# Kernel optimization log

Hardware: AMD Instinct MI355X
Metric: run time of the kernel (lower is better)

## Reference

```python
import jax, jax.numpy as jnp
import numpy as np

N = 50000
E = 800000
G = 256          # number of graphs in the batch
F_IN = 128
H1, D1 = 12, 32  # conv1: heads, out-per-head (concat -> 384)
H2, D2 = 1, 64   # conv2: single head
NEG_SLOPE = 0.2


def setup_inputs() -> dict:
    key = jax.random.key(0)
    ks = jax.random.split(key, 12)
    x = jax.random.normal(ks[0], (N, F_IN), dtype=jnp.float32)
    edge_index = jax.random.randint(ks[1], (2, E), 0, N, dtype=jnp.int64)
    batch = jnp.sort(jax.random.randint(ks[2], (N,), 0, G, dtype=jnp.int64))
    # conv1 params (Glorot-ish scaling)
    W1 = jax.random.normal(ks[3], (F_IN, H1 * D1), dtype=jnp.float32) * (1.0 / np.sqrt(F_IN))
    att_src1 = jax.random.normal(ks[4], (H1, D1), dtype=jnp.float32) * (1.0 / np.sqrt(D1))
    att_dst1 = jax.random.normal(ks[5], (H1, D1), dtype=jnp.float32) * (1.0 / np.sqrt(D1))
    bias1 = jnp.zeros((H1 * D1,), dtype=jnp.float32)
    # conv2 params
    W2 = jax.random.normal(ks[6], (H1 * D1, H2 * D2), dtype=jnp.float32) * (1.0 / np.sqrt(H1 * D1))
    att_src2 = jax.random.normal(ks[7], (H2, D2), dtype=jnp.float32) * (1.0 / np.sqrt(D2))
    att_dst2 = jax.random.normal(ks[8], (H2, D2), dtype=jnp.float32) * (1.0 / np.sqrt(D2))
    bias2 = jnp.zeros((H2 * D2,), dtype=jnp.float32)
    return {"x": x, "edge_index": edge_index, "batch": batch,
            "W1": W1, "att_src1": att_src1, "att_dst1": att_dst1, "bias1": bias1,
            "W2": W2, "att_src2": att_src2, "att_dst2": att_dst2, "bias2": bias2}


def gat_conv(x, src, dst, W, att_src, att_dst, bias, heads, d_out):
    # x: [N, F] -> h: [N, heads, d_out]
    h = (x @ W).reshape(N, heads, d_out)
    # per-node attention halves: [N, heads]
    a_src = jnp.einsum('nhd,hd->nh', h, att_src)
    a_dst = jnp.einsum('nhd,hd->nh', h, att_dst)
    # per-edge logits (edges include self-loops): [Etot, heads]
    e = jax.nn.leaky_relu(a_src[src] + a_dst[dst], NEG_SLOPE)
    # segment softmax over incoming edges of each destination node
    m = jax.ops.segment_max(e, dst, num_segments=N)          # [N, heads]
    e = jnp.exp(e - m[dst])
    s = jax.ops.segment_sum(e, dst, num_segments=N)          # [N, heads]
    alpha = e / s[dst]
    # weighted aggregation: [N, heads, d_out]
    out = jax.ops.segment_sum(alpha[:, :, None] * h[src], dst, num_segments=N)
    return out.reshape(N, heads * d_out) + bias


def reference(x, edge_index, batch, W1, att_src1, att_dst1, bias1,
              W2, att_src2, att_dst2, bias2):
    # add self-loops (PyG GATConv default add_self_loops=True)
    loops = jnp.arange(N, dtype=edge_index.dtype)
    src = jnp.concatenate([edge_index[0], loops])
    dst = jnp.concatenate([edge_index[1], loops])

    h = jax.nn.relu(gat_conv(x, src, dst, W1, att_src1, att_dst1, bias1, H1, D1))
    h = gat_conv(h, src, dst, W2, att_src2, att_dst2, bias2, H2, D2)

    # global mean pool over graphs
    sums = jax.ops.segment_sum(h, batch, num_segments=G)                 # [G, 64]
    cnts = jax.ops.segment_sum(jnp.ones((N,), h.dtype), batch, num_segments=G)
    return sums / jnp.maximum(cnts, 1.0)[:, None]
```

## Files before the change

### kernel.cpp

```cpp
#include <hip/hip_runtime.h>

#define N_NODES 50000
#define N_EDGES 800000
#define ETOT (N_EDGES + N_NODES)
#define G_GRAPHS 256
#define F_IN 128
#define H1 12
#define D1 32
#define C1 (H1*D1)
#define C2 64
#define NEG 0.2f
#define SCAN_B 1024
#define NBLK_SCAN ((N_NODES + SCAN_B - 1)/SCAN_B)

using bf16x8  = __attribute__((ext_vector_type(8))) short;
using ushort8 = __attribute__((ext_vector_type(8))) unsigned short;
using f32x4   = __attribute__((ext_vector_type(4))) float;

__device__ __forceinline__ float lrelu(float x){ return x > 0.f ? x : NEG*x; }
__device__ __forceinline__ unsigned short f2bf(float f){
  unsigned u = __float_as_uint(f);
  u += 0x7fffu + ((u >> 16) & 1u);
  return (unsigned short)(u >> 16);
}
__device__ __forceinline__ float bf2f(unsigned short h){
  return __uint_as_float(((unsigned)h) << 16);
}

__global__ void cast_x_kernel(const float* __restrict__ x, unsigned short* __restrict__ xb){
  int i = blockIdx.x*blockDim.x + threadIdx.x;
  int base = i*4;
  if (base >= N_NODES*F_IN) return;
  float4 v = *(const float4*)(x + base);
  ushort4 o; o.x=f2bf(v.x); o.y=f2bf(v.y); o.z=f2bf(v.z); o.w=f2bf(v.w);
  *(ushort4*)(xb + base) = o;
}
__global__ void transpose_w_kernel(const float* __restrict__ W, unsigned short* __restrict__ Wt,
                                   int K, int Nc){
  int i = blockIdx.x*blockDim.x + threadIdx.x;
  if (i >= K*Nc) return;
  int n = i / K, k = i % K;
  Wt[i] = f2bf(W[(size_t)k*Nc + n]);
}
__global__ void wab_prep(const float* __restrict__ W1, const float* __restrict__ att_src,
                         const float* __restrict__ att_dst, unsigned short* __restrict__ wAb){
  int i = blockIdx.x*blockDim.x + threadIdx.x;
  if (i >= 32*F_IN) return;
  int c = i >> 7, k = i & 127;
  float v = 0.f;
  if (c < 12){
    #pragma unroll
    for (int dd=0; dd<D1; ++dd) v += W1[(size_t)k*C1 + c*D1 + dd] * att_src[c*D1 + dd];
  } else if (c < 24){
    int h = c - 12;
    #pragma unroll
    for (int dd=0; dd<D1; ++dd) v += W1[(size_t)k*C1 + h*D1 + dd] * att_dst[h*D1 + dd];
  }
  wAb[i] = f2bf(v);
}

template<int BM,int BN,int WM,int WN,bool F32OUT>
__global__ __launch_bounds__(256) void gemm_mfma(const unsigned short* __restrict__ A,
    const unsigned short* __restrict__ Bt, void* __restrict__ Cv,
    int M, int N, int K){
  constexpr int BK = 32;
  __shared__ unsigned short As2[4][BM][8];
  __shared__ unsigned short Bs2[4][BN][8];
  const int tid  = threadIdx.x;
  const int wid  = tid >> 6, lane = tid & 63;
  constexpr int NWX = BN / WN;
  const int wrow = (wid / NWX) * WM, wcol = (wid % NWX) * WN;
  constexpr int MR = WM/16, NR = WN/16;
  const int row0 = blockIdx.x * BM, col0 = blockIdx.y * BN;
  const int r = lane & 15, koct = lane >> 4;
  f32x4 acc[MR][NR];
  #pragma unroll
  for (int m=0;m<MR;m++)
    #pragma unroll
    for (int n=0;n<NR;n++) acc[m][n] = f32x4{0.f,0.f,0.f,0.f};

  for (int k0 = 0; k0 < K; k0 += BK){
    for (int s = tid; s < BM*8; s += 256){
      int rr = s >> 3, cc = (s & 7) * 4;
      int gr = row0 + rr;
      ushort4 v = (gr < M) ? *(const ushort4*)(A + (size_t)gr*K + k0 + cc)
                           : ushort4{0,0,0,0};
      *(ushort4*)(&As2[cc>>3][rr][cc&7]) = v;
    }
    for (int s = tid; s < BN*8; s += 256){
      int rr = s >> 3, cc = (s & 7) * 4;
      ushort4 v = *(const ushort4*)(Bt + (size_t)(col0+rr)*K + k0 + cc);
      *(ushort4*)(&Bs2[cc>>3][rr][cc&7]) = v;
    }
    __syncthreads();
    bf16x8 af[MR], bq[NR];
    #pragma unroll
    for (int m=0;m<MR;m++) af[m] = *(const bf16x8*)(&As2[koct][wrow + m*16 + r][0]);
    #pragma unroll
    for (int n=0;n<NR;n++) bq[n] = *(const bf16x8*)(&Bs2[koct][wcol + n*16 + r][0]);
    #pragma unroll
    for (int m=0;m<MR;m++)
      #pragma unroll
      for (int n=0;n<NR;n++)
        acc[m][n] = __builtin_amdgcn_mfma_f32_16x16x32_bf16(af[m], bq[n], acc[m][n], 0,0,0);
    __syncthreads();
  }
  #pragma unroll
  for (int m=0;m<MR;m++){
    #pragma unroll
    for (int rr=0; rr<4; rr++){
      int grow = row0 + wrow + m*16 + koct*4 + rr;
      if (grow < M){
        #pragma unroll
        for (int n=0;n<NR;n++){
          if constexpr (F32OUT)
            ((float*)Cv)[(size_t)grow*N + col0 + wcol + n*16 + r] = acc[m][n][rr];
          else
            ((unsigned short*)Cv)[(size_t)grow*N + col0 + wcol + n*16 + r] = f2bf(acc[m][n][rr]);
        }
      }
    }
  }
}

__global__ void count_kernel(const int* __restrict__ ei, int* __restrict__ counts){
  int e = blockIdx.x*blockDim.x + threadIdx.x;
  if (e >= ETOT) return;
  int d = (e < N_EDGES) ? ei[N_EDGES + e] : (e - N_EDGES);
  atomicAdd(&counts[d], 1);
}
__global__ __launch_bounds__(SCAN_B) void scan_pass1(const int* __restrict__ counts,
    int* __restrict__ excl, int* __restrict__ bsum){
  __shared__ int sdata[SCAN_B];
  int i = blockIdx.x*SCAN_B + threadIdx.x;
  int v = (i < N_NODES) ? counts[i] : 0;
  sdata[threadIdx.x] = v;
  __syncthreads();
  for (int off=1; off<SCAN_B; off<<=1){
    int t = (threadIdx.x >= off) ? sdata[threadIdx.x-off] : 0;
    __syncthreads();
    sdata[threadIdx.x] += t;
    __syncthreads();
  }
  if (i < N_NODES) excl[i] = sdata[threadIdx.x] - v;
  if (threadIdx.x == SCAN_B-1) bsum[blockIdx.x] = sdata[SCAN_B-1];
}
__global__ void scan_pass2(int* __restrict__ bsum){
  if (threadIdx.x == 0){
    int acc = 0;
    for (int b=0;b<NBLK_SCAN;b++){ int t = bsum[b]; bsum[b] = acc; acc += t; }
  }
}
__global__ void scan_pass3(int* __restrict__ rowptr, const int* __restrict__ bsum,
                           int* __restrict__ cursor){
  int i = blockIdx.x*blockDim.x + threadIdx.x;
  if (i < N_NODES){
    int r = rowptr[i] + bsum[i/SCAN_B];
    rowptr[i] = r; cursor[i] = r;
  }
  if (i == N_NODES) rowptr[N_NODES] = ETOT;
}
__global__ void scatter_kernel(const int* __restrict__ ei, int* __restrict__ cursor,
                               int* __restrict__ csr_src){
  int e = blockIdx.x*blockDim.x + threadIdx.x;
  if (e >= ETOT) return;
  int s, d;
  if (e < N_EDGES){ s = ei[e]; d = ei[N_EDGES + e]; } else { s = d = e - N_EDGES; }
  int slot = atomicAdd(&cursor[d], 1);
  csr_src[slot] = s;
}

__global__ __launch_bounds__(64) void alpha1_kernel(const int* __restrict__ rowptr,
    const int* __restrict__ csr, const float* __restrict__ asd,
    float* __restrict__ alpha){
  int d = blockIdx.x, lane = threadIdx.x;
  int r0 = rowptr[d], r1 = rowptr[d+1], deg = r1 - r0;
  float4 ad0 = *(const float4*)(asd + (size_t)d*32 + 12);
  float4 ad1 = *(const float4*)(asd + (size_t)d*32 + 16);
  float4 ad2 = *(const float4*)(asd + (size_t)d*32 + 20);
  float ad[12] = {ad0.x,ad0.y,ad0.z,ad0.w, ad1.x,ad1.y,ad1.z,ad1.w, ad2.x,ad2.y,ad2.z,ad2.w};

  if (deg <= 64){
    bool act = lane < deg;
    int j = r0 + lane;
    int s = act ? csr[j] : 0;
    float4 s0 = *(const float4*)(asd + (size_t)s*32);
    float4 s1 = *(const float4*)(asd + (size_t)s*32 + 4);
    float4 s2 = *(const float4*)(asd + (size_t)s*32 + 8);
    float as[12] = {s0.x,s0.y,s0.z,s0.w, s1.x,s1.y,s1.z,s1.w, s2.x,s2.y,s2.z,s2.w};
    float w[12];
    #pragma unroll
    for (int h=0; h<12; ++h){
      float l = act ? lrelu(as[h] + ad[h]) : -1e30f;
      float m = l;
      #pragma unroll
      for (int off=32; off; off>>=1) m = fmaxf(m, __shfl_xor(m, off));
      float wv = act ? __expf(l - m) : 0.f;
      float ss = wv;
      #pragma unroll
      for (int off=32; off; off>>=1) ss += __shfl_xor(ss, off);
      w[h] = wv / ss;
    }
    if (act){
      float4 o0 = {w[0],w[1],w[2],w[3]};
      float4 o1 = {w[4],w[5],w[6],w[7]};
      float4 o2 = {w[8],w[9],w[10],w[11]};
      *(float4*)(alpha + (size_t)j*12)     = o0;
      *(float4*)(alpha + (size_t)j*12 + 4) = o1;
      *(float4*)(alpha + (size_t)j*12 + 8) = o2;
    }
  } else {
    float mx[12], ss[12];
    #pragma unroll
    for (int h=0;h<12;h++){ mx[h] = -1e30f; ss[h] = 0.f; }
    for (int j = r0 + lane; j < r1; j += 64){
      int s = csr[j];
      float4 s0 = *(const float4*)(asd + (size_t)s*32);
      float4 s1 = *(const float4*)(asd + (size_t)s*32 + 4);
      float4 s2 = *(const float4*)(asd + (size_t)s*32 + 8);
      float as[12] = {s0.x,s0.y,s0.z,s0.w, s1.x,s1.y,s1.z,s1.w, s2.x,s2.y,s2.z,s2.w};
      #pragma unroll
      for (int h=0;h<12;h++) mx[h] = fmaxf(mx[h], lrelu(as[h] + ad[h]));
    }
    #pragma unroll
    for (int h=0;h<12;h++){
      #pragma unroll
      for (int off=32; off; off>>=1) mx[h] = fmaxf(mx[h], __shfl_xor(mx[h], off));
    }
    for (int j = r0 + lane; j < r1; j += 64){
      int s = csr[j];
      float4 s0 = *(const float4*)(asd + (size_t)s*32);
      float4 s1 = *(const float4*)(asd + (size_t)s*32 + 4);
      float4 s2 = *(const float4*)(asd + (size_t)s*32 + 8);
      float as[12] = {s0.x,s0.y,s0.z,s0.w, s1.x,s1.y,s1.z,s1.w, s2.x,s2.y,s2.z,s2.w};
      float w[12];
      #pragma unroll
      for (int h=0;h<12;h++){ w[h] = __expf(lrelu(as[h]+ad[h]) - mx[h]); ss[h] += w[h]; }
      float4 o0 = {w[0],w[1],w[2],w[3]};
      float4 o1 = {w[4],w[5],w[6],w[7]};
      float4 o2 = {w[8],w[9],w[10],w[11]};
      *(float4*)(alpha + (size_t)j*12)     = o0;
      *(float4*)(alpha + (size_t)j*12 + 4) = o1;
      *(float4*)(alpha + (size_t)j*12 + 8) = o2;
    }
    float inv[12];
    #pragma unroll
    for (int h=0;h<12;h++){
      #pragma unroll
      for (int off=32; off; off>>=1) ss[h] += __shfl_xor(ss[h], off);
      inv[h] = 1.f / ss[h];
    }
    for (int j = r0 + lane; j < r1; j += 64){
      float4 o0 = *(const float4*)(alpha + (size_t)j*12);
      float4 o1 = *(const float4*)(alpha + (size_t)j*12 + 4);
      float4 o2 = *(const float4*)(alpha + (size_t)j*12 + 8);
      o0.x*=inv[0]; o0.y*=inv[1]; o0.z*=inv[2]; o0.w*=inv[3];
      o1.x*=inv[4]; o1.y*=inv[5]; o1.z*=inv[6]; o1.w*=inv[7];
      o2.x*=inv[8]; o2.y*=inv[9]; o2.z*=inv[10]; o2.w*=inv[11];
      *(float4*)(alpha + (size_t)j*12)     = o0;
      *(float4*)(alpha + (size_t)j*12 + 4) = o1;
      *(float4*)(alpha + (size_t)j*12 + 8) = o2;
    }
  }
}

__global__ __launch_bounds__(256) void agg1x_kernel(const int* __restrict__ rowptr,
    const int* __restrict__ csr, const unsigned short* __restrict__ xb,
    const float* __restrict__ alpha, const unsigned short* __restrict__ w1t,
    const float* __restrict__ bias, unsigned short* __restrict__ out1){
  constexpr int ROWE = 6*F_IN + 8;
  __shared__ unsigned short agg[16*ROWE];
  int tid = threadIdx.x;
  int g = tid >> 4, t16 = tid & 15;
  int d = blockIdx.x*16 + g;
  int r0 = rowptr[d], r1 = rowptr[d+1];
  float acc[12][8];
  #pragma unroll
  for (int h=0;h<12;h++)
    #pragma unroll
    for (int i=0;i<8;i++) acc[h][i] = 0.f;

  float4 a0={0,0,0,0}, a1={0,0,0,0}, a2={0,0,0,0};
  ushort8 xv = {0,0,0,0,0,0,0,0};
  if (r0 < r1){
    int s = csr[r0];
    a0 = *(const float4*)(alpha + (size_t)r0*12);
    a1 = *(const float4*)(alpha + (size_t)r0*12 + 4);
    a2 = *(const float4*)(alpha + (size_t)r0*12 + 8);
    xv = *(const ushort8*)(xb + (size_t)s*F_IN + t16*8);
  }
  for (int j = r0; j < r1; ++j){
    float4 c0=a0, c1=a1, c2=a2; ushort8 cx=xv;
    if (j+1 < r1){
      int s = csr[j+1];
      a0 = *(const float4*)(alpha + (size_t)(j+1)*12);
      a1 = *(const float4*)(alpha + (size_t)(j+1)*12 + 4);
      a2 = *(const float4*)(alpha + (size_t)(j+1)*12 + 8);
      xv = *(const ushort8*)(xb + (size_t)s*F_IN + t16*8);
    }
    float xf[8];
    #pragma unroll
    for (int i=0;i<8;i++) xf[i] = bf2f((unsigned short)cx[i]);
    float aw[12] = {c0.x,c0.y,c0.z,c0.w, c1.x,c1.y,c1.z,c1.w, c2.x,c2.y,c2.z,c2.w};
    #pragma unroll
    for (int h=0;h<12;h++)
      #pragma unroll
      for (int i=0;i<8;i++) acc[h][i] += aw[h]*xf[i];
  }

  int wid = tid >> 6, lane = tid & 63;
  int r = lane & 15, q = lane >> 4;
  #pragma unroll
  for (int half = 0; half < 2; ++half){
    if (half) __syncthreads();
    #pragma unroll
    for (int h = 0; h < 6; ++h){
      ushort8 v;
      #pragma unroll
      for (int i=0;i<8;i++) v[i] = f2bf(acc[half*6+h][i]);
      *(ushort8*)(&agg[g*ROWE + h*F_IN + t16*8]) = v;
    }
    __syncthreads();
    for (int t = wid; t < 12; t += 4){
      int h = t >> 1, nb = t & 1;
      int hh = half*6 + h;
      f32x4 c = {0.f,0.f,0.f,0.f};
      #pragma unroll
      for (int kk=0; kk<4; ++kk){
        bf16x8 af = *(const bf16x8*)(&agg[r*ROWE + h*F_IN + kk*32 + q*8]);
        bf16x8 bq = *(const bf16x8*)(w1t + (size_t)(hh*32 + nb*16 + r)*F_IN + kk*32 + q*8);
        c = __builtin_amdgcn_mfma_f32_16x16x32_bf16(af, bq, c, 0,0,0);
      }
      int col = hh*32 + nb*16 + r;
      float bv = bias[col];
      #pragma unroll
      for (int rr=0; rr<4; ++rr){
        int od = blockIdx.x*16 + q*4 + rr;
        out1[(size_t)od*C1 + col] = f2bf(fmaxf(c[rr] + bv, 0.f));
      }
    }
  }
}

__global__ void a2_kernel(const unsigned short* __restrict__ h2,
    const float* __restrict__ att_src, const float* __restrict__ att_dst,
    float* __restrict__ a_src, float* __restrict__ a_dst){
  int n = blockIdx.x*blockDim.x + threadIdx.x;
  if (n >= N_NODES) return;
  const unsigned short* hp = h2 + (size_t)n*C2;
  float s=0.f, d=0.f;
  #pragma unroll
  for (int k4=0;k4<16;k4++){
    ushort4 v = *(const ushort4*)(hp + k4*4);
    int b = k4*4;
    s += bf2f(v.x)*att_src[b] + bf2f(v.y)*att_src[b+1] + bf2f(v.z)*att_src[b+2] + bf2f(v.w)*att_src[b+3];
    d += bf2f(v.x)*att_dst[b] + bf2f(v.y)*att_dst[b+1] + bf2f(v.z)*att_dst[b+2] + bf2f(v.w)*att_dst[b+3];
  }
  a_src[n]=s; a_dst[n]=d;
}

#define AGG2_CH 64
__global__ __launch_bounds__(64) void agg2f_kernel(const int* __restrict__ rowptr,
    const int* __restrict__ csr, const unsigned short* __restrict__ h2,
    const float* __restrict__ asrc, const float* __restrict__ adst,
    const float* __restrict__ bias, const int* __restrict__ batch,
    float* __restrict__ pool){
  int d = blockIdx.x, tid = threadIdx.x;
  int r0 = rowptr[d], r1 = rowptr[d+1];
  float ad = adst[d];
  float m = -1e30f, ss = 0.f;
  for (int j = r0 + tid; j < r1; j += 64){
    float l = lrelu(asrc[csr[j]] + ad);
    float mn = fmaxf(m, l);
    ss = ss*__expf(m - mn) + __expf(l - mn);
    m = mn;
  }
  #pragma unroll
  for (int off=32; off; off>>=1){
    float m2 = __shfl_xor(m, off);
    float s2 = __shfl_xor(ss, off);
    float mn = fmaxf(m, m2);
    ss = ss*__expf(m - mn) + s2*__expf(m2 - mn);
    m = mn;
  }
  float inv = 1.f / ss;
  __shared__ int   s_lds[AGG2_CH];
  __shared__ float red[3][C2];
  int grp = tid >> 4;
  int fb  = (tid & 15) * 4;
  float a0=0.f, a1=0.f, a2=0.f, a3=0.f;
  for (int c0 = r0; c0 < r1; c0 += AGG2_CH){
    int nc = min(AGG2_CH, r1 - c0);
    __syncthreads();
    if (tid < nc) s_lds[tid] = csr[c0 + tid];
    __syncthreads();
    for (int e = grp; e < nc; e += 4){
      int s = s_lds[e];
      float w = __expf(lrelu(asrc[s] + ad) - m);
      ushort4 hv = *(const ushort4*)(h2 + (size_t)s*C2 + fb);
      a0 += w*bf2f(hv.x); a1 += w*bf2f(hv.y); a2 += w*bf2f(hv.z); a3 += w*bf2f(hv.w);
    }
  }
  __syncthreads();
  if (grp > 0){
    float* p = &red[grp-1][fb];
    p[0]=a0; p[1]=a1; p[2]=a2; p[3]=a3;
  }
  __syncthreads();
  if (grp == 0){
    int g = batch[d];
    float4 b4 = *(const float4*)(bias + fb);
    float v0 = (a0 + red[0][fb+0] + red[1][fb+0] + red[2][fb+0])*inv + b4.x;
    float v1 = (a1 + red[0][fb+1] + red[1][fb+1] + red[2][fb+1])*inv + b4.y;
    float v2 = (a2 + red[0][fb+2] + red[1][fb+2] + red[2][fb+2])*inv + b4.z;
    float v3 = (a3 + red[0][fb+3] + red[1][fb+3] + red[2][fb+3])*inv + b4.w;
    atomicAdd(&pool[g*C2 + fb+0], v0);
    atomicAdd(&pool[g*C2 + fb+1], v1);
    atomicAdd(&pool[g*C2 + fb+2], v2);
    atomicAdd(&pool[g*C2 + fb+3], v3);
  }
}

__global__ void cnt_kernel(const int* __restrict__ batch, int* __restrict__ cnt){
  int n = blockIdx.x*blockDim.x + threadIdx.x;
  if (n < N_NODES) atomicAdd(&cnt[batch[n]], 1);
}
__global__ void finalize_kernel(const float* __restrict__ sums, const int* __restrict__ cnt,
                                float* __restrict__ out){
  int i = blockIdx.x*blockDim.x + threadIdx.x;
  if (i >= G_GRAPHS*C2) return;
  int g = i >> 6;
  out[i] = sums[i] / fmaxf((float)cnt[g], 1.f);
}

extern "C" void kernel_launch(void* const* d_in, const int* in_sizes, int n_in,
                              void* d_out, int out_size, void* d_ws, size_t ws_size,
                              hipStream_t stream) {
  const float* x        = (const float*)d_in[0];
  const int*   ei       = (const int*)  d_in[1];
  const int*   batch    = (const int*)  d_in[2];
  const float* W1       = (const float*)d_in[3];
  const float* att_src1 = (const float*)d_in[4];
  const float* att_dst1 = (const float*)d_in[5];
  const float* bias1    = (const float*)d_in[6];
  const float* W2       = (const float*)d_in[7];
  const float* att_src2 = (const float*)d_in[8];
  const float* att_dst2 = (const float*)d_in[9];
  const float* bias2    = (const float*)d_in[10];
  float* out = (float*)d_out;

  char* ws = (char*)d_ws;
  size_t o = 0;
  auto alloc = [&](size_t bytes)->size_t{ size_t r=o; o=(o+bytes+255)&~(size_t)255; return r; };

  size_t xb_o     = alloc((size_t)N_NODES*F_IN*2);
  size_t w1t_o    = alloc((size_t)C1*F_IN*2);
  size_t w2t_o    = alloc((size_t)C2*C1*2);
  size_t wab_o    = alloc((size_t)32*F_IN*2);
  size_t asd_o    = alloc((size_t)N_NODES*32*4);
  size_t out1_o   = alloc((size_t)N_NODES*C1*2);
  size_t h2_o     = alloc((size_t)N_NODES*C2*2);
  size_t asrc2_o  = alloc((size_t)N_NODES*4);
  size_t adst2_o  = alloc((size_t)N_NODES*4);
  size_t alpha1_o = alloc((size_t)ETOT*H1*4);
  size_t zero_beg = o;
  size_t counts_o = alloc((size_t)N_NODES*4);
  size_t pool_o   = alloc((size_t)G_GRAPHS*C2*4);
  size_t cnt_o    = alloc((size_t)G_GRAPHS*4);
  size_t zero_end = o;
  size_t rowptr_o = alloc((size_t)(N_NODES+1)*4);
  size_t bsum_o   = alloc((size_t)NBLK_SCAN*4);
  size_t cursor_o = alloc((size_t)N_NODES*4);
  size_t csr_o    = alloc((size_t)ETOT*4);

  unsigned short* xb    = (unsigned short*)(ws + xb_o);
  unsigned short* w1t   = (unsigned short*)(ws + w1t_o);
  unsigned short* w2t   = (unsigned short*)(ws + w2t_o);
  unsigned short* wab   = (unsigned short*)(ws + wab_o);
  float* asd    = (float*)(ws + asd_o);
  unsigned short* out1b = (unsigned short*)(ws + out1_o);
  unsigned short* h2b   = (unsigned short*)(ws + h2_o);
  float* asrc2  = (float*)(ws + asrc2_o);
  float* adst2  = (float*)(ws + adst2_o);
  float* alpha1 = (float*)(ws + alpha1_o);
  int*   counts = (int*)  (ws + counts_o);
  float* poolf  = (float*)(ws + pool_o);
  int*   cnt    = (int*)  (ws + cnt_o);
  int*   rowptr = (int*)  (ws + rowptr_o);
  int*   bsum   = (int*)  (ws + bsum_o);
  int*   cursor = (int*)  (ws + cursor_o);
  int*   csrsrc = (int*)  (ws + csr_o);

  hipMemsetAsync(ws + zero_beg, 0, zero_end - zero_beg, stream);

  const int TPB = 256;
  int egrid = (ETOT + TPB - 1)/TPB;

  cast_x_kernel<<<(N_NODES*F_IN/4 + TPB-1)/TPB, TPB, 0, stream>>>(x, xb);
  transpose_w_kernel<<<(F_IN*C1 + TPB-1)/TPB, TPB, 0, stream>>>(W1, w1t, F_IN, C1);
  transpose_w_kernel<<<(C1*C2 + TPB-1)/TPB, TPB, 0, stream>>>(W2, w2t, C1, C2);
  wab_prep<<<(32*F_IN + TPB-1)/TPB, TPB, 0, stream>>>(W1, att_src1, att_dst1, wab);

  count_kernel<<<egrid, TPB, 0, stream>>>(ei, counts);
  scan_pass1<<<NBLK_SCAN, SCAN_B, 0, stream>>>(counts, rowptr, bsum);
  scan_pass2<<<1, 64, 0, stream>>>(bsum);
  scan_pass3<<<(N_NODES + TPB)/TPB, TPB, 0, stream>>>(rowptr, bsum, cursor);
  scatter_kernel<<<egrid, TPB, 0, stream>>>(ei, cursor, csrsrc);

  gemm_mfma<128,32,32,32,true><<<dim3((N_NODES+127)/128, 1), 256, 0, stream>>>(xb, wab, asd, N_NODES, 32, F_IN);
  alpha1_kernel<<<N_NODES, 64, 0, stream>>>(rowptr, csrsrc, asd, alpha1);
  agg1x_kernel<<<N_NODES/16, 256, 0, stream>>>(rowptr, csrsrc, xb, alpha1, w1t, bias1, out1b);

  gemm_mfma<128,64,64,32,false><<<dim3((N_NODES+127)/128, 1), 256, 0, stream>>>(out1b, w2t, h2b, N_NODES, C2, C1);
  a2_kernel<<<(N_NODES + TPB-1)/TPB, TPB, 0, stream>>>(h2b, att_src2, att_dst2, asrc2, adst2);
  agg2f_kernel<<<N_NODES, 64, 0, stream>>>(rowptr, csrsrc, h2b, asrc2, adst2, bias2, batch, poolf);

  cnt_kernel<<<(N_NODES + TPB-1)/TPB, TPB, 0, stream>>>(batch, cnt);
  finalize_kernel<<<(G_GRAPHS*C2 + TPB-1)/TPB, TPB, 0, stream>>>(poolf, cnt, out);
}
```

Before: 510.2 us.

## Fuse layer-1 softmax weights into aggregation kernel, dropping alpha buffer

Merges the separate per-edge softmax kernel into the layer-1 aggregation kernel. Each destination node now gets a 32-lane half-wave that computes the max, then produces unnormalized exp weights in LDS chunks of 16 edges. The two 16-lane groups each process alternate edges and are combined by a shuffle, with the 1/sum normalization applied before the MFMA projection. This removes the write and re-read of the ETOT x 12 float alpha array and one kernel launch. In exchange, each edge's source scores are gathered twice and register pressure rises with 512-thread blocks.

```diff
diff --git a/kernel.cpp b/kernel.cpp
--- a/kernel.cpp
+++ b/kernel.cpp
@@ -170,172 +170,140 @@
   csr_src[slot] = s;
 }
 
-__global__ __launch_bounds__(64) void alpha1_kernel(const int* __restrict__ rowptr,
-    const int* __restrict__ csr, const float* __restrict__ asd,
-    float* __restrict__ alpha){
-  int d = blockIdx.x, lane = threadIdx.x;
-  int r0 = rowptr[d], r1 = rowptr[d+1], deg = r1 - r0;
+__global__ __launch_bounds__(512) void agg1f_kernel(const int* __restrict__ rowptr,
+    const int* __restrict__ csr, const unsigned short* __restrict__ xb,
+    const float* __restrict__ asd, const unsigned short* __restrict__ w1t,
+    const float* __restrict__ bias, unsigned short* __restrict__ out1){
+  constexpr int ROWE = 6*F_IN + 8;
+  __shared__ unsigned short agg[16*ROWE];
+  __shared__ float wlds[16][16*12];
+  __shared__ int   slds[16][16];
+
+  const int tid  = threadIdx.x;
+  const int wv   = tid >> 6;
+  const int lane = tid & 63;
+  const int half = lane >> 5;
+  const int t    = lane & 31;
+  const int eh   = t >> 4;
+  const int t16  = t & 15;
+  const int slot = wv*2 + half;
+  const int d    = blockIdx.x*16 + slot;
+  const int r0 = rowptr[d], r1 = rowptr[d+1];
+
   float4 ad0 = *(const float4*)(asd + (size_t)d*32 + 12);
   float4 ad1 = *(const float4*)(asd + (size_t)d*32 + 16);
   float4 ad2 = *(const float4*)(asd + (size_t)d*32 + 20);
   float ad[12] = {ad0.x,ad0.y,ad0.z,ad0.w, ad1.x,ad1.y,ad1.z,ad1.w, ad2.x,ad2.y,ad2.z,ad2.w};
 
-  if (deg <= 64){
-    bool act = lane < deg;
-    int j = r0 + lane;
-    int s = act ? csr[j] : 0;
+  float mx[12];
+  #pragma unroll
+  for (int h=0;h<12;h++) mx[h] = -1e30f;
+  for (int j = r0 + t; j < r1; j += 32){
+    int s = csr[j];
     float4 s0 = *(const float4*)(asd + (size_t)s*32);
     float4 s1 = *(const float4*)(asd + (size_t)s*32 + 4);
     float4 s2 = *(const float4*)(asd + (size_t)s*32 + 8);
     float as[12] = {s0.x,s0.y,s0.z,s0.w, s1.x,s1.y,s1.z,s1.w, s2.x,s2.y,s2.z,s2.w};
-    float w[12];
-    #pragma unroll
-    for (int h=0; h<12; ++h){
-      float l = act ? lrelu(as[h] + ad[h]) : -1e30f;
-      float m = l;
-      #pragma unroll
-      for (int off=32; off; off>>=1) m = fmaxf(m, __shfl_xor(m, off));
-      float wv = act ? __expf(l - m) : 0.f;
-      float ss = wv;
-      #pragma unroll
-      for (int off=32; off; off>>=1) ss += __shfl_xor(ss, off);
-      w[h] = wv / ss;
-    }
-    if (act){
-      float4 o0 = {w[0],w[1],w[2],w[3]};
-      float4 o1 = {w[4],w[5],w[6],w[7]};
-      float4 o2 = {w[8],w[9],w[10],w[11]};
-      *(float4*)(alpha + (size_t)j*12)     = o0;
-      *(float4*)(alpha + (size_t)j*12 + 4) = o1;
-      *(float4*)(alpha + (size_t)j*12 + 8) = o2;
-    }
-  } else {
-    float mx[12], ss[12];
-    #pragma unroll
-    for (int h=0;h<12;h++){ mx[h] = -1e30f; ss[h] = 0.f; }
-    for (int j = r0 + lane; j < r1; j += 64){
-      int s = csr[j];
-      float4 s0 = *(const float4*)(asd + (size_t)s*32);
-      float4 s1 = *(const float4*)(asd + (size_t)s*32 + 4);
-      float4 s2 = *(const float4*)(asd + (size_t)s*32 + 8);
-      float as[12] = {s0.x,s0.y,s0.z,s0.w, s1.x,s1.y,s1.z,s1.w, s2.x,s2.y,s2.z,s2.w};
-      #pragma unroll
-      for (int h=0;h<12;h++) mx[h] = fmaxf(mx[h], lrelu(as[h] + ad[h]));
-    }
-    #pragma unroll
-    for (int h=0;h<12;h++){
-      #pragma unroll
-      for (int off=32; off; off>>=1) mx[h] = fmaxf(mx[h], __shfl_xor(mx[h], off));
-    }
-    for (int j = r0 + lane; j < r1; j += 64){
-      int s = csr[j];
+    #pragma unroll
+    for (int h=0;h<12;h++) mx[h] = fmaxf(mx[h], lrelu(as[h] + ad[h]));
+  }
+  #pragma unroll
+  for (int h=0;h<12;h++){
+    #pragma unroll
+    for (int off=16; off; off>>=1) mx[h] = fmaxf(mx[h], __shfl_xor(mx[h], off));
+  }
+
+  float acc[12][8];
+  #pragma unroll
+  for (int h=0;h<12;h++)
+    #pragma unroll
+    for (int i=0;i<8;i++) acc[h][i] = 0.f;
+  float ssp[12];
+  #pragma unroll
+  for (int h=0;h<12;h++) ssp[h] = 0.f;
+
+  for (int c0 = r0; c0 < r1; c0 += 16){
+    int nc = min(16, r1 - c0);
+    if (t < nc){
+      int s = csr[c0 + t];
+      slds[slot][t] = s;
       float4 s0 = *(const float4*)(asd + (size_t)s*32);
       float4 s1 = *(const float4*)(asd + (size_t)s*32 + 4);
       float4 s2 = *(const float4*)(asd + (size_t)s*32 + 8);
       float as[12] = {s0.x,s0.y,s0.z,s0.w, s1.x,s1.y,s1.z,s1.w, s2.x,s2.y,s2.z,s2.w};
       float w[12];
       #pragma unroll
-      for (int h=0;h<12;h++){ w[h] = __expf(lrelu(as[h]+ad[h]) - mx[h]); ss[h] += w[h]; }
-      float4 o0 = {w[0],w[1],w[2],w[3]};
-      float4 o1 = {w[4],w[5],w[6],w[7]};
-      float4 o2 = {w[8],w[9],w[10],w[11]};
-      *(float4*)(alpha + (size_t)j*12)     = o0;
-      *(float4*)(alpha + (size_t)j*12 + 4) = o1;
-      *(float4*)(alpha + (size_t)j*12 + 8) = o2;
-    }
-    float inv[12];
-    #pragma unroll
-    for (int h=0;h<12;h++){
-      #pragma unroll
-      for (int off=32; off; off>>=1) ss[h] += __shfl_xor(ss[h], off);
-      inv[h] = 1.f / ss[h];
-    }
-    for (int j = r0 + lane; j < r1; j += 64){
-      float4 o0 = *(const float4*)(alpha + (size_t)j*12);
-      float4 o1 = *(const float4*)(alpha + (size_t)j*12 + 4);
-      float4 o2 = *(const float4*)(alpha + (size_t)j*12 + 8);
-      o0.x*=inv[0]; o0.y*=inv[1]; o0.z*=inv[2]; o0.w*=inv[3];
-      o1.x*=inv[4]; o1.y*=inv[5]; o1.z*=inv[6]; o1.w*=inv[7];
-      o2.x*=inv[8]; o2.y*=inv[9]; o2.z*=inv[10]; o2.w*=inv[11];
-      *(float4*)(alpha + (size_t)j*12)     = o0;
-      *(float4*)(alpha + (size_t)j*12 + 4) = o1;
-      *(float4*)(alpha + (size_t)j*12 + 8) = o2;
-    }
-  }
-}
-
-__global__ __launch_bounds__(256) void agg1x_kernel(const int* __restrict__ rowptr,
-    const int* __restrict__ csr, const unsigned short* __restrict__ xb,
-    const float* __restrict__ alpha, const unsigned short* __restrict__ w1t,
-    const float* __restrict__ bias, unsigned short* __restrict__ out1){
-  constexpr int ROWE = 6*F_IN + 8;
-  __shared__ unsigned short agg[16*ROWE];
-  int tid = threadIdx.x;
-  int g = tid >> 4, t16 = tid & 15;
-  int d = blockIdx.x*16 + g;
-  int r0 = rowptr[d], r1 = rowptr[d+1];
-  float acc[12][8];
+      for (int h=0;h<12;h++){ w[h] = __expf(lrelu(as[h] + ad[h]) - mx[h]); ssp[h] += w[h]; }
+      *(float4*)(&wlds[slot][t*12 + 0]) = float4{w[0],w[1],w[2],w[3]};
+      *(float4*)(&wlds[slot][t*12 + 4]) = float4{w[4],w[5],w[6],w[7]};
+      *(float4*)(&wlds[slot][t*12 + 8]) = float4{w[8],w[9],w[10],w[11]};
+    }
+    __builtin_amdgcn_wave_barrier();
+    for (int e0 = 0; e0 < nc; e0 += 2){
+      int e = e0 + eh;
+      bool valid = e < nc;
+      int ee = valid ? e : 0;
+      int s = slds[slot][ee];
+      float4 w0 = *(const float4*)(&wlds[slot][ee*12 + 0]);
+      float4 w1 = *(const float4*)(&wlds[slot][ee*12 + 4]);
+      float4 w2 = *(const float4*)(&wlds[slot][ee*12 + 8]);
+      if (!valid){ w0 = float4{0,0,0,0}; w1 = float4{0,0,0,0}; w2 = float4{0,0,0,0}; }
+      ushort8 cx = *(const ushort8*)(xb + (size_t)s*F_IN + t16*8);
+      float xf[8];
+      #pragma unroll
+      for (int i=0;i<8;i++) xf[i] = bf2f((unsigned short)cx[i]);
+      float w[12] = {w0.x,w0.y,w0.z,w0.w, w1.x,w1.y,w1.z,w1.w, w2.x,w2.y,w2.z,w2.w};
+      #pragma unroll
+      for (int h=0;h<12;h++)
+        #pragma unroll
+        for (int i=0;i<8;i++) acc[h][i] += w[h]*xf[i];
+    }
+    __builtin_amdgcn_wave_barrier();
+  }
+
+  #pragma unroll
+  for (int h=0;h<12;h++){
+    #pragma unroll
+    for (int off=16; off; off>>=1) ssp[h] += __shfl_xor(ssp[h], off);
+  }
   #pragma unroll
   for (int h=0;h<12;h++)
     #pragma unroll
-    for (int i=0;i<8;i++) acc[h][i] = 0.f;
-
-  float4 a0={0,0,0,0}, a1={0,0,0,0}, a2={0,0,0,0};
-  ushort8 xv = {0,0,0,0,0,0,0,0};
-  if (r0 < r1){
-    int s = csr[r0];
-    a0 = *(const float4*)(alpha + (size_t)r0*12);
-    a1 = *(const float4*)(alpha + (size_t)r0*12 + 4);
-    a2 = *(const float4*)(alpha + (size_t)r0*12 + 8);
-    xv = *(const ushort8*)(xb + (size_t)s*F_IN + t16*8);
-  }
-  for (int j = r0; j < r1; ++j){
-    float4 c0=a0, c1=a1, c2=a2; ushort8 cx=xv;
-    if (j+1 < r1){
-      int s = csr[j+1];
-      a0 = *(const float4*)(alpha + (size_t)(j+1)*12);
-      a1 = *(const float4*)(alpha + (size_t)(j+1)*12 + 4);
-      a2 = *(const float4*)(alpha + (size_t)(j+1)*12 + 8);
-      xv = *(const ushort8*)(xb + (size_t)s*F_IN + t16*8);
-    }
-    float xf[8];
-    #pragma unroll
-    for (int i=0;i<8;i++) xf[i] = bf2f((unsigned short)cx[i]);
-    float aw[12] = {c0.x,c0.y,c0.z,c0.w, c1.x,c1.y,c1.z,c1.w, c2.x,c2.y,c2.z,c2.w};
-    #pragma unroll
-    for (int h=0;h<12;h++)
-      #pragma unroll
-      for (int i=0;i<8;i++) acc[h][i] += aw[h]*xf[i];
-  }
-
-  int wid = tid >> 6, lane = tid & 63;
-  int r = lane & 15, q = lane >> 4;
-  #pragma unroll
-  for (int half = 0; half < 2; ++half){
-    if (half) __syncthreads();
-    #pragma unroll
-    for (int h = 0; h < 6; ++h){
-      ushort8 v;
-      #pragma unroll
-      for (int i=0;i<8;i++) v[i] = f2bf(acc[half*6+h][i]);
-      *(ushort8*)(&agg[g*ROWE + h*F_IN + t16*8]) = v;
-    }
-    __syncthreads();
-    for (int t = wid; t < 12; t += 4){
-      int h = t >> 1, nb = t & 1;
-      int hh = half*6 + h;
+    for (int i=0;i<8;i++) acc[h][i] += __shfl_xor(acc[h][i], 16);
+  float inv[12];
+  #pragma unroll
+  for (int h=0;h<12;h++) inv[h] = 1.f / ssp[h];
+
+  const int er = lane & 15, eq = lane >> 4;
+  #pragma unroll
+  for (int hf = 0; hf < 2; ++hf){
+    __syncthreads();
+    if (eh == 0){
+      #pragma unroll
+      for (int h = 0; h < 6; ++h){
+        int hh = hf*6 + h;
+        ushort8 v;
+        #pragma unroll
+        for (int i=0;i<8;i++) v[i] = f2bf(acc[hh][i]*inv[hh]);
+        *(ushort8*)(&agg[slot*ROWE + h*F_IN + t16*8]) = v;
+      }
+    }
+    __syncthreads();
+    for (int tt = wv; tt < 12; tt += 8){
+      int h = tt >> 1, nb = tt & 1;
+      int hh = hf*6 + h;
       f32x4 c = {0.f,0.f,0.f,0.f};
       #pragma unroll
       for (int kk=0; kk<4; ++kk){
-        bf16x8 af = *(const bf16x8*)(&agg[r*ROWE + h*F_IN + kk*32 + q*8]);
-        bf16x8 bq = *(const bf16x8*)(w1t + (size_t)(hh*32 + nb*16 + r)*F_IN + kk*32 + q*8);
+        bf16x8 af = *(const bf16x8*)(&agg[er*ROWE + h*F_IN + kk*32 + eq*8]);
+        bf16x8 bq = *(const bf16x8*)(w1t + (size_t)(hh*32 + nb*16 + er)*F_IN + kk*32 + eq*8);
         c = __builtin_amdgcn_mfma_f32_16x16x32_bf16(af, bq, c, 0,0,0);
       }
-      int col = hh*32 + nb*16 + r;
+      int col = hh*32 + nb*16 + er;
       float bv = bias[col];
       #pragma unroll
       for (int rr=0; rr<4; ++rr){
-        int od = blockIdx.x*16 + q*4 + rr;
+        int od = blockIdx.x*16 + eq*4 + rr;
         out1[(size_t)od*C1 + col] = f2bf(fmaxf(c[rr] + bv, 0.f));
       }
     }
@@ -462,7 +430,6 @@
   size_t h2_o     = alloc((size_t)N_NODES*C2*2);
   size_t asrc2_o  = alloc((size_t)N_NODES*4);
   size_t adst2_o  = alloc((size_t)N_NODES*4);
-  size_t alpha1_o = alloc((size_t)ETOT*H1*4);
   size_t zero_beg = o;
   size_t counts_o = alloc((size_t)N_NODES*4);
   size_t pool_o   = alloc((size_t)G_GRAPHS*C2*4);
@@ -482,7 +449,6 @@
   unsigned short* h2b   = (unsigned short*)(ws + h2_o);
   float* asrc2  = (float*)(ws + asrc2_o);
   float* adst2  = (float*)(ws + adst2_o);
-  float* alpha1 = (float*)(ws + alpha1_o);
   int*   counts = (int*)  (ws + counts_o);
   float* poolf  = (float*)(ws + pool_o);
   int*   cnt    = (int*)  (ws + cnt_o);
@@ -508,8 +474,7 @@
   scatter_kernel<<<egrid, TPB, 0, stream>>>(ei, cursor, csrsrc);
 
   gemm_mfma<128,32,32,32,true><<<dim3((N_NODES+127)/128, 1), 256, 0, stream>>>(xb, wab, asd, N_NODES, 32, F_IN);
-  alpha1_kernel<<<N_NODES, 64, 0, stream>>>(rowptr, csrsrc, asd, alpha1);
-  agg1x_kernel<<<N_NODES/16, 256, 0, stream>>>(rowptr, csrsrc, xb, alpha1, w1t, bias1, out1b);
+  agg1f_kernel<<<N_NODES/16, 512, 0, stream>>>(rowptr, csrsrc, xb, asd, w1t, bias1, out1b);
 
   gemm_mfma<128,64,64,32,false><<<dim3((N_NODES+127)/128, 1), 256, 0, stream>>>(out1b, w2t, h2b, N_NODES, C2, C1);
   a2_kernel<<<(N_NODES + TPB-1)/TPB, TPB, 0, stream>>>(h2b, att_src2, att_dst2, asrc2, adst2);
```

Result: slower. 531.5 us (+4.2%).

## Pack multiple nodes per block and use online softmax in layer-2 aggregation

Applied to the files above, without the earlier changes.

alpha1 and the layer-2 aggregation now process four destination nodes per 256-thread block instead of one node per 64-thread block. Layer-2 aggregation becomes a single-pass online softmax with one feature per lane, dropping the separate max/sum pass, the LDS staging and the cross-group reduction. Layer-1 aggregation assigns 32 lanes per node with half the per-thread accumulators and a 512-thread block, to cut register pressure and raise occupancy. The GEMM tile configurations are also shrunk to launch more blocks. The sequential per-edge loop in layer 2 carries a dependent exp chain, which may limit latency hiding on high-degree nodes.

```diff
diff --git a/kernel.cpp b/kernel.cpp
--- a/kernel.cpp
+++ b/kernel.cpp
@@ -170,10 +170,11 @@
   csr_src[slot] = s;
 }
 
-__global__ __launch_bounds__(64) void alpha1_kernel(const int* __restrict__ rowptr,
+__global__ __launch_bounds__(256) void alpha1_kernel(const int* __restrict__ rowptr,
     const int* __restrict__ csr, const float* __restrict__ asd,
     float* __restrict__ alpha){
-  int d = blockIdx.x, lane = threadIdx.x;
+  int d = blockIdx.x*4 + (threadIdx.x >> 6);
+  int lane = threadIdx.x & 63;
   int r0 = rowptr[d], r1 = rowptr[d+1], deg = r1 - r0;
   float4 ad0 = *(const float4*)(asd + (size_t)d*32 + 12);
   float4 ad1 = *(const float4*)(asd + (size_t)d*32 + 16);
@@ -202,12 +203,9 @@
       w[h] = wv / ss;
     }
     if (act){
-      float4 o0 = {w[0],w[1],w[2],w[3]};
-      float4 o1 = {w[4],w[5],w[6],w[7]};
-      float4 o2 = {w[8],w[9],w[10],w[11]};
-      *(float4*)(alpha + (size_t)j*12)     = o0;
-      *(float4*)(alpha + (size_t)j*12 + 4) = o1;
-      *(float4*)(alpha + (size_t)j*12 + 8) = o2;
+      *(float4*)(alpha + (size_t)j*12)     = float4{w[0],w[1],w[2],w[3]};
+      *(float4*)(alpha + (size_t)j*12 + 4) = float4{w[4],w[5],w[6],w[7]};
+      *(float4*)(alpha + (size_t)j*12 + 8) = float4{w[8],w[9],w[10],w[11]};
     }
   } else {
     float mx[12], ss[12];
@@ -236,12 +234,9 @@
       float w[12];
       #pragma unroll
       for (int h=0;h<12;h++){ w[h] = __expf(lrelu(as[h]+ad[h]) - mx[h]); ss[h] += w[h]; }
-      float4 o0 = {w[0],w[1],w[2],w[3]};
-      float4 o1 = {w[4],w[5],w[6],w[7]};
-      float4 o2 = {w[8],w[9],w[10],w[11]};
-      *(float4*)(alpha + (size_t)j*12)     = o0;
-      *(float4*)(alpha + (size_t)j*12 + 4) = o1;
-      *(float4*)(alpha + (size_t)j*12 + 8) = o2;
+      *(float4*)(alpha + (size_t)j*12)     = float4{w[0],w[1],w[2],w[3]};
+      *(float4*)(alpha + (size_t)j*12 + 4) = float4{w[4],w[5],w[6],w[7]};
+      *(float4*)(alpha + (size_t)j*12 + 8) = float4{w[8],w[9],w[10],w[11]};
     }
     float inv[12];
     #pragma unroll
@@ -264,78 +259,81 @@
   }
 }
 
-__global__ __launch_bounds__(256) void agg1x_kernel(const int* __restrict__ rowptr,
+__global__ __launch_bounds__(512) void agg1x2_kernel(const int* __restrict__ rowptr,
     const int* __restrict__ csr, const unsigned short* __restrict__ xb,
     const float* __restrict__ alpha, const unsigned short* __restrict__ w1t,
     const float* __restrict__ bias, unsigned short* __restrict__ out1){
   constexpr int ROWE = 6*F_IN + 8;
   __shared__ unsigned short agg[16*ROWE];
-  int tid = threadIdx.x;
-  int g = tid >> 4, t16 = tid & 15;
-  int d = blockIdx.x*16 + g;
-  int r0 = rowptr[d], r1 = rowptr[d+1];
-  float acc[12][8];
+  const int tid  = threadIdx.x;
+  const int wv   = tid >> 6;
+  const int lane = tid & 63;
+  const int half = lane >> 5;
+  const int t    = lane & 31;
+  const int slot = wv*2 + half;
+  const int d    = blockIdx.x*16 + slot;
+  const int r0 = rowptr[d], r1 = rowptr[d+1];
+
+  float acc[12][4];
   #pragma unroll
   for (int h=0;h<12;h++)
     #pragma unroll
-    for (int i=0;i<8;i++) acc[h][i] = 0.f;
+    for (int i=0;i<4;i++) acc[h][i] = 0.f;
 
   float4 a0={0,0,0,0}, a1={0,0,0,0}, a2={0,0,0,0};
-  ushort8 xv = {0,0,0,0,0,0,0,0};
+  ushort4 xv = {0,0,0,0};
   if (r0 < r1){
     int s = csr[r0];
     a0 = *(const float4*)(alpha + (size_t)r0*12);
     a1 = *(const float4*)(alpha + (size_t)r0*12 + 4);
     a2 = *(const float4*)(alpha + (size_t)r0*12 + 8);
-    xv = *(const ushort8*)(xb + (size_t)s*F_IN + t16*8);
+    xv = *(const ushort4*)(xb + (size_t)s*F_IN + t*4);
   }
   for (int j = r0; j < r1; ++j){
-    float4 c0=a0, c1=a1, c2=a2; ushort8 cx=xv;
+    float4 c0=a0, c1=a1, c2=a2; ushort4 cx=xv;
     if (j+1 < r1){
       int s = csr[j+1];
       a0 = *(const float4*)(alpha + (size_t)(j+1)*12);
       a1 = *(const float4*)(alpha + (size_t)(j+1)*12 + 4);
       a2 = *(const float4*)(alpha + (size_t)(j+1)*12 + 8);
-      xv = *(const ushort8*)(xb + (size_t)s*F_IN + t16*8);
-    }
-    float xf[8];
-    #pragma unroll
-    for (int i=0;i<8;i++) xf[i] = bf2f((unsigned short)cx[i]);
-    float aw[12] = {c0.x,c0.y,c0.z,c0.w, c1.x,c1.y,c1.z,c1.w, c2.x,c2.y,c2.z,c2.w};
+      xv = *(const ushort4*)(xb + (size_t)s*F_IN + t*4);
+    }
+    float xf[4] = {bf2f(cx.x), bf2f(cx.y), bf2f(cx.z), bf2f(cx.w)};
+    float w[12] = {c0.x,c0.y,c0.z,c0.w, c1.x,c1.y,c1.z,c1.w, c2.x,c2.y,c2.z,c2.w};
     #pragma unroll
     for (int h=0;h<12;h++)
       #pragma unroll
-      for (int i=0;i<8;i++) acc[h][i] += aw[h]*xf[i];
-  }
-
-  int wid = tid >> 6, lane = tid & 63;
-  int r = lane & 15, q = lane >> 4;
+      for (int i=0;i<4;i++) acc[h][i] += w[h]*xf[i];
+  }
+
+  const int er = lane & 15, eq = lane >> 4;
   #pragma unroll
-  for (int half = 0; half < 2; ++half){
-    if (half) __syncthreads();
+  for (int hf = 0; hf < 2; ++hf){
+    __syncthreads();
     #pragma unroll
     for (int h = 0; h < 6; ++h){
-      ushort8 v;
-      #pragma unroll
-      for (int i=0;i<8;i++) v[i] = f2bf(acc[half*6+h][i]);
-      *(ushort8*)(&agg[g*ROWE + h*F_IN + t16*8]) = v;
-    }
-    __syncthreads();
-    for (int t = wid; t < 12; t += 4){
-      int h = t >> 1, nb = t & 1;
-      int hh = half*6 + h;
+      int hh = hf*6 + h;
+      ushort4 v;
+      v.x = f2bf(acc[hh][0]); v.y = f2bf(acc[hh][1]);
+      v.z = f2bf(acc[hh][2]); v.w = f2bf(acc[hh][3]);
+      *(ushort4*)(&agg[slot*ROWE + h*F_IN + t*4]) = v;
+    }
+    __syncthreads();
+    for (int tt = wv; tt < 12; tt += 8){
+      int h = tt >> 1, nb = tt & 1;
+      int hh = hf*6 + h;
       f32x4 c = {0.f,0.f,0.f,0.f};
       #pragma unroll
       for (int kk=0; kk<4; ++kk){
-        bf16x8 af = *(const bf16x8*)(&agg[r*ROWE + h*F_IN + kk*32 + q*8]);
-        bf16x8 bq = *(const bf16x8*)(w1t + (size_t)(hh*32 + nb*16 + r)*F_IN + kk*32 + q*8);
+        bf16x8 af = *(const bf16x8*)(&agg[er*ROWE + h*F_IN + kk*32 + eq*8]);
+        bf16x8 bq = *(const bf16x8*)(w1t + (size_t)(hh*32 + nb*16 + er)*F_IN + kk*32 + eq*8);
         c = __builtin_amdgcn_mfma_f32_16x16x32_bf16(af, bq, c, 0,0,0);
       }
-      int col = hh*32 + nb*16 + r;
+      int col = hh*32 + nb*16 + er;
       float bv = bias[col];
       #pragma unroll
       for (int rr=0; rr<4; ++rr){
-        int od = blockIdx.x*16 + q*4 + rr;
+        int od = blockIdx.x*16 + eq*4 + rr;
         out1[(size_t)od*C1 + col] = f2bf(fmaxf(c[rr] + bv, 0.f));
       }
     }
@@ -359,66 +357,37 @@
   a_src[n]=s; a_dst[n]=d;
 }
 
-#define AGG2_CH 64
-__global__ __launch_bounds__(64) void agg2f_kernel(const int* __restrict__ rowptr,
+__global__ __launch_bounds__(256) void agg2o_kernel(const int* __restrict__ rowptr,
     const int* __restrict__ csr, const unsigned short* __restrict__ h2,
     const float* __restrict__ asrc, const float* __restrict__ adst,
     const float* __restrict__ bias, const int* __restrict__ batch,
     float* __restrict__ pool){
-  int d = blockIdx.x, tid = threadIdx.x;
+  int d = blockIdx.x*4 + (threadIdx.x >> 6);
+  int lane = threadIdx.x & 63;
   int r0 = rowptr[d], r1 = rowptr[d+1];
   float ad = adst[d];
-  float m = -1e30f, ss = 0.f;
-  for (int j = r0 + tid; j < r1; j += 64){
-    float l = lrelu(asrc[csr[j]] + ad);
+  float m = -1e30f, ss = 0.f, acc = 0.f;
+  int   sN = (r0 < r1) ? csr[r0] : 0;
+  float aN = asrc[sN];
+  float hN = bf2f(h2[(size_t)sN*C2 + lane]);
+  for (int j = r0; j < r1; ++j){
+    float aC = aN, hC = hN;
+    if (j+1 < r1){
+      int s = csr[j+1];
+      aN = asrc[s];
+      hN = bf2f(h2[(size_t)s*C2 + lane]);
+    }
+    float l = lrelu(aC + ad);
     float mn = fmaxf(m, l);
-    ss = ss*__expf(m - mn) + __expf(l - mn);
+    float corr = __expf(m - mn);
+    float w = __expf(l - mn);
+    ss  = ss*corr + w;
+    acc = acc*corr + w*hC;
     m = mn;
   }
-  #pragma unroll
-  for (int off=32; off; off>>=1){
-    float m2 = __shfl_xor(m, off);
-    float s2 = __shfl_xor(ss, off);
-    float mn = fmaxf(m, m2);
-    ss = ss*__expf(m - mn) + s2*__expf(m2 - mn);
-    m = mn;
-  }
-  float inv = 1.f / ss;
-  __shared__ int   s_lds[AGG2_CH];
-  __shared__ float red[3][C2];
-  int grp = tid >> 4;
-  int fb  = (tid & 15) * 4;
-  float a0=0.f, a1=0.f, a2=0.f, a3=0.f;
-  for (int c0 = r0; c0 < r1; c0 += AGG2_CH){
-    int nc = min(AGG2_CH, r1 - c0);
-    __syncthreads();
-    if (tid < nc) s_lds[tid] = csr[c0 + tid];
-    __syncthreads();
-    for (int e = grp; e < nc; e += 4){
-      int s = s_lds[e];
-      float w = __expf(lrelu(asrc[s] + ad) - m);
-      ushort4 hv = *(const ushort4*)(h2 + (size_t)s*C2 + fb);
-      a0 += w*bf2f(hv.x); a1 += w*bf2f(hv.y); a2 += w*bf2f(hv.z); a3 += w*bf2f(hv.w);
-    }
-  }
-  __syncthreads();
-  if (grp > 0){
-    float* p = &red[grp-1][fb];
-    p[0]=a0; p[1]=a1; p[2]=a2; p[3]=a3;
-  }
-  __syncthreads();
-  if (grp == 0){
-    int g = batch[d];
-    float4 b4 = *(const float4*)(bias + fb);
-    float v0 = (a0 + red[0][fb+0] + red[1][fb+0] + red[2][fb+0])*inv + b4.x;
-    float v1 = (a1 + red[0][fb+1] + red[1][fb+1] + red[2][fb+1])*inv + b4.y;
-    float v2 = (a2 + red[0][fb+2] + red[1][fb+2] + red[2][fb+2])*inv + b4.z;
-    float v3 = (a3 + red[0][fb+3] + red[1][fb+3] + red[2][fb+3])*inv + b4.w;
-    atomicAdd(&pool[g*C2 + fb+0], v0);
-    atomicAdd(&pool[g*C2 + fb+1], v1);
-    atomicAdd(&pool[g*C2 + fb+2], v2);
-    atomicAdd(&pool[g*C2 + fb+3], v3);
-  }
+  int g = batch[d];
+  float v = acc/ss + bias[lane];
+  atomicAdd(&pool[g*C2 + lane], v);
 }
 
 __global__ void cnt_kernel(const int* __restrict__ batch, int* __restrict__ cnt){
@@ -507,13 +476,13 @@
   scan_pass3<<<(N_NODES + TPB)/TPB, TPB, 0, stream>>>(rowptr, bsum, cursor);
   scatter_kernel<<<egrid, TPB, 0, stream>>>(ei, cursor, csrsrc);
 
-  gemm_mfma<128,32,32,32,true><<<dim3((N_NODES+127)/128, 1), 256, 0, stream>>>(xb, wab, asd, N_NODES, 32, F_IN);
-  alpha1_kernel<<<N_NODES, 64, 0, stream>>>(rowptr, csrsrc, asd, alpha1);
-  agg1x_kernel<<<N_NODES/16, 256, 0, stream>>>(rowptr, csrsrc, xb, alpha1, w1t, bias1, out1b);
-
-  gemm_mfma<128,64,64,32,false><<<dim3((N_NODES+127)/128, 1), 256, 0, stream>>>(out1b, w2t, h2b, N_NODES, C2, C1);
+  gemm_mfma<64,32,32,16,true><<<dim3((N_NODES+63)/64, 1), 256, 0, stream>>>(xb, wab, asd, N_NODES, 32, F_IN);
+  alpha1_kernel<<<(N_NODES+3)/4, 256, 0, stream>>>(rowptr, csrsrc, asd, alpha1);
+  agg1x2_kernel<<<N_NODES/16, 512, 0, stream>>>(rowptr, csrsrc, xb, alpha1, w1t, bias1, out1b);
+
+  gemm_mfma<64,64,32,32,false><<<dim3((N_NODES+63)/64, 1), 256, 0, stream>>>(out1b, w2t, h2b, N_NODES, C2, C1);
   a2_kernel<<<(N_NODES + TPB-1)/TPB, TPB, 0, stream>>>(h2b, att_src2, att_dst2, asrc2, adst2);
-  agg2f_kernel<<<N_NODES, 64, 0, stream>>>(rowptr, csrsrc, h2b, asrc2, adst2, bias2, batch, poolf);
+  agg2o_kernel<<<(N_NODES+3)/4, 256, 0, stream>>>(rowptr, csrsrc, h2b, asrc2, adst2, bias2, batch, poolf);
 
   cnt_kernel<<<(N_NODES + TPB-1)/TPB, TPB, 0, stream>>>(batch, cnt);
   finalize_kernel<<<(G_GRAPHS*C2 + TPB-1)/TPB, TPB, 0, stream>>>(poolf, cnt, out);
```

Measured after the change: 530.5 us. 1.04x slower.
